# Performance work log

Measured on AMD Instinct MI355X. Metric: run time of the kernel, lower is better.

## Reference

```python
import jax, jax.numpy as jnp
import numpy as np

NUM_HEADS = 12
NUM_GROUPS = 4
METRIC_SCALE = 1.0
CLS_MIX = 1.0
MEAN_MIX = 0.5
ROUTER_SCALE = 1.0
DIFF_SCALE = 1.0
B, N, D, HF = 16, 577, 768, 3072


def _ln(x, g, b, eps=1e-5):
    mu = jnp.mean(x, axis=-1, keepdims=True)
    var = jnp.mean(jnp.square(x - mu), axis=-1, keepdims=True)
    return (x - mu) * jax.lax.rsqrt(var + eps) * g + b


def setup_inputs() -> dict:
    key = jax.random.key(0)
    ks = iter(jax.random.split(key, 16))
    w = lambda shape, std: jax.random.normal(next(ks), shape, jnp.float32) * std
    return {
        "x": w((B, N, D), 1.0),
        "ln1_g": jnp.ones((D,)), "ln1_b": jnp.zeros((D,)),
        "ad_ln_g": jnp.ones((D,)), "ad_ln_b": jnp.zeros((D,)),
        "ad_w": w((D, D), 0.02),
        "w_qkv": w((D, 3 * D), 0.02),
        "w_proj": w((D, D), 0.02), "b_proj": jnp.zeros((D,)),
        "ln2_g": jnp.ones((D,)), "ln2_b": jnp.zeros((D,)),
        "fc1_w": w((D, HF), 0.02), "fc1_b": jnp.zeros((HF,)),
        "fc2_w": w((HF, D), 0.02), "fc2_b": jnp.zeros((D,)),
        "r_ln_g": jnp.ones((HF,)), "r_ln_b": jnp.zeros((HF,)),
        "r_proj_w": w((2 * HF, NUM_GROUPS), 0.02), "r_proj_b": jnp.zeros((NUM_GROUPS,)),
        "r_gate_w": w((2 * HF, 1), 0.02), "r_gate_b": jnp.full((1,), -2.0),
        "r_scale": jnp.full((NUM_GROUPS,), 0.1),
        "d_ln_g": jnp.ones((HF,)), "d_ln_b": jnp.zeros((HF,)),
        "d_out_w": w((HF, HF), 0.005),
        "d_gate_w": w((HF, 1), 0.02), "d_gate_b": jnp.full((1,), -1.5),
    }


def reference(x, ln1_g, ln1_b, ad_ln_g, ad_ln_b, ad_w, w_qkv, w_proj, b_proj,
              ln2_g, ln2_b, fc1_w, fc1_b, fc2_w, fc2_b,
              r_ln_g, r_ln_b, r_proj_w, r_proj_b, r_gate_w, r_gate_b, r_scale,
              d_ln_g, d_ln_b, d_out_w, d_gate_w, d_gate_b):
    b, n, d = x.shape
    hd = d // NUM_HEADS
    # ---- GeoAttention (pre-norm) ----
    h = _ln(x, ln1_g, ln1_b)
    # metric adapter: residual LN+Linear (SharedAttentionMetricAdapter)
    metric_h = h + METRIC_SCALE * (_ln(h, ad_ln_g, ad_ln_b) @ ad_w)
    # q,k from metric path; v from plain path (asymmetric Q/K vs V)
    qk = metric_h @ w_qkv[:, : 2 * d]                # [b,n,2d]
    v = h @ w_qkv[:, 2 * d :]                        # [b,n,d]
    q = qk[..., :d].reshape(b, n, NUM_HEADS, hd).transpose(0, 2, 1, 3)
    k = qk[..., d:].reshape(b, n, NUM_HEADS, hd).transpose(0, 2, 1, 3)
    v = v.reshape(b, n, NUM_HEADS, hd).transpose(0, 2, 1, 3)
    attn = jax.nn.softmax(jnp.einsum("bhnd,bhmd->bhnm", q, k) * (hd ** -0.5), axis=-1)
    out = jnp.einsum("bhnm,bhmd->bhnd", attn, v).transpose(0, 2, 1, 3).reshape(b, n, d)
    x = x + out @ w_proj + b_proj
    # ---- GeoMlp (pre-norm) ----
    h2 = _ln(x, ln2_g, ln2_b)
    hid = h2 @ fc1_w + fc1_b                         # [b,n,HF]
    # GroupCompetitionRouter on hidden
    rn = _ln(hid, r_ln_g, r_ln_b)
    summary = jnp.concatenate([CLS_MIX * rn[:, 0], MEAN_MIX * jnp.mean(rn[:, 1:], axis=1)], axis=-1)  # [b,2HF]
    wts = jax.nn.softmax(summary @ r_proj_w + r_proj_b, axis=-1)       # [b,G]
    gate = jax.nn.sigmoid(summary @ r_gate_w + r_gate_b)               # [b,1]
    centered = wts * float(NUM_GROUPS) - 1.0
    grouped = hid.reshape(b, n, NUM_GROUPS, HF // NUM_GROUPS)
    scale = 1.0 + ROUTER_SCALE * gate[:, None, :, None] * r_scale[None, None, :, None] * centered[:, None, :, None]
    hid = (grouped * scale).reshape(b, n, HF)
    # TokenDiffusionMixer on hidden
    dn = _ln(hid, d_ln_g, d_ln_b)
    tr = dn / jnp.maximum(jnp.linalg.norm(dn, axis=-1, keepdims=True), 1e-12)
    aff = jax.nn.softmax(jnp.einsum("bnc,bmc->bnm", tr, tr) * (HF ** -0.5), axis=-1)
    diffusion = jnp.einsum("bnm,bmc->bnc", aff, dn) - dn
    dgate = jax.nn.sigmoid(dn[:, 0] @ d_gate_w + d_gate_b)             # [b,1]
    hid = hid + DIFF_SCALE * dgate[:, :, None] * (diffusion @ d_out_w)
    # activation + fc2
    hid = jax.nn.gelu(hid, approximate=False)
    return x + hid @ fc2_w + fc2_b
```

## Files before the change

kernel.cpp:

```cpp
#include <hip/hip_runtime.h>
#include <math.h>

typedef unsigned short u16;
typedef unsigned int   u32;
typedef __attribute__((ext_vector_type(4))) float f32x4;
typedef __attribute__((ext_vector_type(4))) u32   u32x4;
typedef __attribute__((ext_vector_type(8))) short s16x8;

#define DEV __device__ __forceinline__
#define AS1 __attribute__((address_space(1)))
#define AS3 __attribute__((address_space(3)))

DEV float b2f(u16 u){ u32 x = ((u32)u)<<16; float f; __builtin_memcpy(&f,&x,4); return f; }
DEV u16 f2b(float f){ u32 x; __builtin_memcpy(&x,&f,4); u32 r = x + 0x7FFFu + ((x>>16)&1u); return (u16)(r>>16); }

DEV float ldf(const float* p, long i){ return p[i]; }
DEV float ldf(const u16*   p, long i){ return b2f(p[i]); }

DEV void gload16(const u16* g, u16* l){
  __builtin_amdgcn_global_load_lds((const AS1 u32*)(const void*)g,
                                   (AS3 u32*)(void*)l, 16, 0, 0);
}

DEV float wave_sum(float v){
#pragma unroll
  for(int o=32;o;o>>=1) v += __shfl_down(v,o,64);
  return v;
}
DEV float wave_max(float v){
#pragma unroll
  for(int o=32;o;o>>=1) v = fmaxf(v, __shfl_down(v,o,64));
  return v;
}
DEV float block_sum(float v, float* tmp){
  v = wave_sum(v);
  if((threadIdx.x&63)==0) tmp[threadIdx.x>>6]=v;
  __syncthreads();
  float r = tmp[0]+tmp[1]+tmp[2]+tmp[3];
  __syncthreads();
  return r;
}
DEV float block_max(float v, float* tmp){
  v = wave_max(v);
  if((threadIdx.x&63)==0) tmp[threadIdx.x>>6]=v;
  __syncthreads();
  float r = fmaxf(fmaxf(tmp[0],tmp[1]),fmaxf(tmp[2],tmp[3]));
  __syncthreads();
  return r;
}

template<typename TI>
__global__ void transpose_pad(const TI* __restrict__ in, u16* __restrict__ out,
                              int R, int C, int Rpad, long strideI, long strideO){
  __shared__ u16 t[32][33];
  in  += (long)blockIdx.z*strideI;
  out += (long)blockIdx.z*strideO;
  int tx = threadIdx.x & 31, ty = threadIdx.x >> 5;
  int bc = blockIdx.x*32, br = blockIdx.y*32;
#pragma unroll
  for(int i=0;i<32;i+=8){
    int r = br+ty+i, c = bc+tx;
    float v = (r<R && c<C) ? ldf(in,(long)r*C+c) : 0.f;
    t[ty+i][tx] = f2b(v);
  }
  __syncthreads();
#pragma unroll
  for(int i=0;i<32;i+=8){
    int c = bc+ty+i, r = br+tx;
    if(c<C && r<Rpad) out[(long)c*Rpad + r] = t[tx][ty+i];
  }
}

template<typename TI>
__global__ void ln_rows(const TI* __restrict__ x, const float* __restrict__ g,
                        const float* __restrict__ b, u16* __restrict__ y, int W){
  __shared__ float tmp[4];
  long base=(long)blockIdx.x*W;
  float s=0.f, ss=0.f;
  for(int c=threadIdx.x;c<W;c+=256){ float v=ldf(x,base+c); s+=v; ss+=v*v; }
  s=block_sum(s,tmp); ss=block_sum(ss,tmp);
  float mu=s/W;
  float rstd=rsqrtf(fmaxf(ss/W-mu*mu,0.f)+1e-5f);
  for(int c=threadIdx.x;c<W;c+=256){
    float v=ldf(x,base+c);
    y[base+c]=f2b((v-mu)*rstd*g[c]+b[c]);
  }
}

__global__ void row_stats(const u16* __restrict__ x, float* __restrict__ stats, int W){
  __shared__ float tmp[4];
  long base=(long)blockIdx.x*W;
  float s=0.f,ss=0.f;
  for(int c=threadIdx.x;c<W;c+=256){ float v=b2f(x[base+c]); s+=v; ss+=v*v; }
  s=block_sum(s,tmp); ss=block_sum(ss,tmp);
  if(threadIdx.x==0){
    float mu=s/W;
    stats[2*(long)blockIdx.x]=mu;
    stats[2*(long)blockIdx.x+1]=rsqrtf(fmaxf(ss/W-mu*mu,0.f)+1e-5f);
  }
}

__global__ void dn_kernel(const u16* __restrict__ x, const float* __restrict__ g,
                          const float* __restrict__ b, const float* __restrict__ scalef,
                          u16* __restrict__ dn, float* __restrict__ rn){
  const int W=3072;
  __shared__ float tmp[4];
  __shared__ u16 rowb[3072];
  long row=(long)blockIdx.x;
  long base=row*(long)W;
  int bz=(int)(row/577);
  float s=0.f,ss=0.f;
  for(int c=threadIdx.x;c<W;c+=256){
    float sc=scalef[bz*4 + ((c>>8)/3)];
    float v=b2f(x[base+c])*sc;
    rowb[c]=f2b(v);
    s+=v; ss+=v*v;
  }
  s=block_sum(s,tmp); ss=block_sum(ss,tmp);
  float mu=s/W;
  float rstd=rsqrtf(fmaxf(ss/W-mu*mu,0.f)+1e-5f);
  float sq=0.f;
  for(int c=threadIdx.x;c<W;c+=256){
    float v=(b2f(rowb[c])-mu)*rstd*g[c]+b[c];
    sq+=v*v;
  }
  sq=block_sum(sq,tmp);
  float r=1.f/fmaxf(sqrtf(sq),1e-12f);
  for(int c=threadIdx.x;c<W;c+=256){
    float v=(b2f(rowb[c])-mu)*rstd*g[c]+b[c];
    dn[base+c]=f2b(v);
  }
  if(threadIdx.x==0) rn[blockIdx.x]=r;
}

__global__ void softmax_rows(u16* __restrict__ S, int W, int Wp,
                             const float* __restrict__ rs, int rpb, float alpha){
  __shared__ float tmp[4];
  long row = blockIdx.x;
  u16* p = S + row*(long)Wp;
  float rowscale = alpha;
  const float* rsb = nullptr;
  if(rs){ long bt=row/rpb; int m=(int)(row%rpb); rsb = rs + bt*(long)rpb; rowscale *= rsb[m]; }
  float mx=-3e38f;
  for(int c=threadIdx.x;c<W;c+=256){
    float v=b2f(p[c])*rowscale; if(rs) v*=rsb[c];
    mx=fmaxf(mx,v);
  }
  mx=block_max(mx,tmp);
  float sm=0.f;
  for(int c=threadIdx.x;c<W;c+=256){
    float v=b2f(p[c])*rowscale; if(rs) v*=rsb[c];
    sm+=__expf(v-mx);
  }
  sm=block_sum(sm,tmp);
  float inv=1.f/sm;
  for(int c=threadIdx.x;c<W;c+=256){
    float v=b2f(p[c])*rowscale; if(rs) v*=rsb[c];
    p[c]=f2b(__expf(v-mx)*inv);
  }
  for(int c=W+threadIdx.x;c<Wp;c+=256) p[c]=0;
}

__global__ void split_heads(const u16* __restrict__ qk, u16* __restrict__ qh, u16* __restrict__ kh){
  int i = blockIdx.x*256+threadIdx.x;
  if(i >= 16*577*12*8) return;
  int dv = i&7; int h=(i>>3)%12; int bn=i/96;
  int b=bn/577, n=bn%577;
  long src=(long)bn*1536 + h*64 + dv*8;
  long dst=((long)((b*12+h)*577+n))*64 + dv*8;
  *(u32x4*)(qh+dst) = *(const u32x4*)(qk+src);
  *(u32x4*)(kh+dst) = *(const u32x4*)(qk+src+768);
}
__global__ void merge_heads(const u16* __restrict__ aoh, u16* __restrict__ aout){
  int i = blockIdx.x*256+threadIdx.x;
  if(i >= 16*577*12*8) return;
  int dv=i&7; int h=(i>>3)%12; int bn=i/96;
  int b=bn/577, n=bn%577;
  long dst=(long)bn*768 + h*64 + dv*8;
  long src=((long)((b*12+h)*577+n))*64 + dv*8;
  *(u32x4*)(aout+dst) = *(const u32x4*)(aoh+src);
}
__global__ void make_vT(const u16* __restrict__ v, u16* __restrict__ vT){
  long i = (long)blockIdx.x*256+threadIdx.x;
  if(i >= (long)192*64*608) return;
  int n=(int)(i%608); long q=i/608; int d=(int)(q&63); int bh=(int)(q>>6);
  int b=bh/12, h=bh%12;
  u16 val=0;
  if(n<577) val = v[((long)(b*577+n))*768 + h*64 + d];
  vT[i]=val;
}

__global__ void summary_kernel(const u16* __restrict__ hid, const float* __restrict__ stats,
                               const float* __restrict__ rg, const float* __restrict__ rb,
                               float* __restrict__ summ){
  int b=blockIdx.y;
  int c=blockIdx.x*256+threadIdx.x;
  const u16* hb=hid+(size_t)b*577*3072;
  const float* st=stats+(size_t)b*577*2;
  float g=rg[c], be=rb[c];
  float cls=(b2f(hb[c])-st[0])*st[1]*g+be;
  float acc=0.f;
  for(int n=1;n<577;n++) acc += (b2f(hb[(size_t)n*3072+c])-st[2*n])*st[2*n+1];
  summ[(size_t)b*6144+c]        = 1.0f*cls;
  summ[(size_t)b*6144+3072+c]   = 0.5f*(g*(acc*(1.f/576.f))+be);
}

__global__ void router_kernel(const float* __restrict__ summ, const float* __restrict__ pw,
                              const float* __restrict__ pb, const float* __restrict__ gw,
                              const float* __restrict__ gb, const float* __restrict__ rsc,
                              float* __restrict__ scalef){
  __shared__ float tmp[4];
  int b=blockIdx.x;
  float a0=0,a1=0,a2=0,a3=0,a4=0;
  for(int c=threadIdx.x;c<6144;c+=256){
    float sv=summ[(size_t)b*6144+c];
    a0+=sv*pw[c*4+0]; a1+=sv*pw[c*4+1]; a2+=sv*pw[c*4+2]; a3+=sv*pw[c*4+3];
    a4+=sv*gw[c];
  }
  a0=block_sum(a0,tmp); a1=block_sum(a1,tmp); a2=block_sum(a2,tmp);
  a3=block_sum(a3,tmp); a4=block_sum(a4,tmp);
  if(threadIdx.x==0){
    float l0=a0+pb[0], l1=a1+pb[1], l2=a2+pb[2], l3=a3+pb[3];
    float mx=fmaxf(fmaxf(l0,l1),fmaxf(l2,l3));
    float e0=__expf(l0-mx),e1=__expf(l1-mx),e2=__expf(l2-mx),e3=__expf(l3-mx);
    float s=e0+e1+e2+e3;
    float gate=1.f/(1.f+__expf(-(a4+gb[0])));
    float w0=e0/s,w1=e1/s,w2=e2/s,w3=e3/s;
    scalef[b*4+0]=1.f+gate*rsc[0]*(4.f*w0-1.f);
    scalef[b*4+1]=1.f+gate*rsc[1]*(4.f*w1-1.f);
    scalef[b*4+2]=1.f+gate*rsc[2]*(4.f*w2-1.f);
    scalef[b*4+3]=1.f+gate*rsc[3]*(4.f*w3-1.f);
  }
}

__global__ void dgate_kernel(const u16* __restrict__ dn, const float* __restrict__ gw,
                             const float* __restrict__ gb, float* __restrict__ dgate){
  __shared__ float tmp[4];
  int b=blockIdx.x;
  const u16* row = dn + (size_t)b*577*3072;
  float a=0.f;
  for(int c=threadIdx.x;c<3072;c+=256) a+=b2f(row[c])*gw[c];
  a=block_sum(a,tmp);
  if(threadIdx.x==0) dgate[b]=1.f/(1.f+__expf(-(a+gb[0])));
}

constexpr int F_BIAS=1, F_RES=2, F_GELU=4, F_GATE=8, F_RESF32=16, F_OUTF32=32, F_SCRES=64;

DEV int swz(int u){ int row=u>>2, sl=u&3; return row*4 + (sl ^ ((row>>1)&3)); }

template<int FLAGS>
__global__ __launch_bounds__(256,2) void gemm_bt(
  const u16* __restrict__ A, long lda, long szA,
  const u16* __restrict__ B, long ldb, long szB,
  void* __restrict__ Cv, long ldc, long szC,
  const float* __restrict__ bias,
  const void* __restrict__ resv, long ldr, long szR, float res_scale,
  const float* __restrict__ gate,
  float alpha, int M, int N, int K, int NX, int NY)
{
  __shared__ alignas(16) u16 shA[128*32];
  __shared__ alignas(16) u16 shB[128*32];
  const int nwg = (int)gridDim.x;
  const int orig = (int)blockIdx.x;
  const int q = nwg>>3, r = nwg&7;
  const int xcd = orig&7, idx = orig>>3;
  const int wg = (xcd<r ? xcd*(q+1) : r*(q+1)+(xcd-r)*q) + idx;
  const int by = wg % NY; const int t_ = wg / NY;
  const int bx = t_ % NX; const int z  = t_ / NX;

  A += (long)z*szA; B += (long)z*szB;
  const int tid=threadIdx.x, lane=tid&63, wid=tid>>6;
  const int wr=wid>>1, wc=wid&1;
  const long m0=(long)bx*128, n0=(long)by*128;
  f32x4 acc[4][4];
#pragma unroll
  for(int i=0;i<4;i++)
#pragma unroll
    for(int j=0;j<4;j++){ f32x4 zv={0.f,0.f,0.f,0.f}; acc[i][j]=zv; }

  const int lr = lane>>2, lsl = lane&3;
  const u16* pA[2]; const u16* pB[2]; u16* lA[2]; u16* lB[2];
#pragma unroll
  for(int i=0;i<2;i++){
    int ra = wid*32 + i*16 + lr;
    int kc = (lsl ^ ((ra>>1)&3))*8;
    long gr = m0+ra; if(gr>=M) gr=M-1;
    long gb = n0+ra; if(gb>=N) gb=N-1;
    pA[i] = A + gr*lda + kc;
    pB[i] = B + gb*ldb + kc;
    lA[i] = shA + (wid*32 + i*16)*32;
    lB[i] = shB + (wid*32 + i*16)*32;
  }

  for(int k0=0;k0<K;k0+=32){
    __syncthreads();
#pragma unroll
    for(int i=0;i<2;i++){
      gload16(pA[i]+k0, lA[i]);
      gload16(pB[i]+k0, lB[i]);
    }
    __syncthreads();
    const int ks = lane>>4, rr = lane&15;
    s16x8 av[4], bv[4];
#pragma unroll
    for(int mi=0;mi<4;mi++) av[mi] = ((const s16x8*)shA)[swz((wr*64+mi*16+rr)*4+ks)];
#pragma unroll
    for(int ni=0;ni<4;ni++) bv[ni] = ((const s16x8*)shB)[swz((wc*64+ni*16+rr)*4+ks)];
#pragma unroll
    for(int mi=0;mi<4;mi++)
#pragma unroll
      for(int ni=0;ni<4;ni++)
        acc[mi][ni] = __builtin_amdgcn_mfma_f32_16x16x32_bf16(av[mi], bv[ni], acc[mi][ni], 0,0,0);
  }
  const float* resf = (const float*)resv + (long)z*szR;
  const u16*   resh = (const u16*)resv   + (long)z*szR;
  float* Cf = (float*)Cv + (long)z*szC;
  u16*   Ch = (u16*)Cv   + (long)z*szC;
  float gv = (FLAGS&F_GATE)? gate[z] : 1.f;
#pragma unroll
  for(int mi=0;mi<4;mi++){
#pragma unroll
    for(int ni=0;ni<4;ni++){
      long c0 = n0 + wc*64 + ni*16 + (lane&15);
      if(c0>=N) continue;
      float bb = (FLAGS&F_BIAS)? bias[c0] : 0.f;
#pragma unroll
      for(int r2=0;r2<4;r2++){
        long rw = m0 + wr*64 + mi*16 + (lane>>4)*4 + r2;
        if(rw>=M) continue;
        float t = acc[mi][ni][r2]*alpha*gv + bb;
        if(FLAGS&F_RES){
          float rvv = (FLAGS&F_RESF32)? resf[rw*ldr+c0] : b2f(resh[rw*ldr+c0]);
          t += res_scale*rvv;
        }
        if(FLAGS&F_GELU) t = 0.5f*t*(1.f+erff(t*0.70710678118654752f));
        if(FLAGS&F_OUTF32) Cf[rw*ldc+c0]=t;
        else               Ch[rw*ldc+c0]=f2b(t);
      }
    }
  }
}

static inline int gpack(int M,int N,int nb,int& NX,int& NY){
  NX=(M+127)/128; NY=(N+127)/128; return NX*NY*nb;
}

template<int FLAGS>
__global__ __launch_bounds__(512,2) void gemm256(
  const u16* __restrict__ A, long lda,
  const u16* __restrict__ B, long ldb,
  void* __restrict__ Cv, long ldc,
  const float* __restrict__ bias,
  const void* __restrict__ resv, long ldr,
  const float* __restrict__ gate, const float* __restrict__ scres,
  float irpz, float alpha, int M, int N, int K, int NY)
{
  __shared__ alignas(16) u16 smem[65536];
  char* sm=(char*)smem;
  const int nwg=(int)gridDim.x, orig=(int)blockIdx.x;
  const int qq=nwg>>3, rr8=nwg&7, xcd=orig&7, idx=orig>>3;
  const int wg=(xcd<rr8? xcd*(qq+1): rr8*(qq+1)+(xcd-rr8)*qq)+idx;
  const int by=wg%NY, bx=wg/NY;
  const long m0=(long)bx*256, n0=(long)by*256;
  const int tid=threadIdx.x, lane=tid&63, wid=tid>>6;
  const int wr=wid>>2, wc=wid&3, l15=lane&15, ks=lane>>4;

  f32x4 acc[8][4];
#pragma unroll
  for(int i=0;i<8;i++)
#pragma unroll
    for(int j=0;j<4;j++){ f32x4 zv={0.f,0.f,0.f,0.f}; acc[i][j]=zv; }

  const u16 *sA[2][2], *sB[2][2];
  int dstj[2];
#pragma unroll
  for(int j=0;j<2;j++){
    int u=j*512+tid, row=u>>3;
    long co=(long)(((u&7)^(row&7))*8);
    dstj[j]=u*16;
#pragma unroll
    for(int h=0;h<2;h++){
      long gr=m0+h*128+row; if(gr>=M) gr=M-1;
      long gb=n0+h*128+row; if(gb>=N) gb=N-1;
      sA[h][j]=A+gr*lda+co;
      sB[h][j]=B+gb*ldb+co;
    }
  }
  int xsl[2]; xsl[0]=((ks^(l15&7))<<4); xsl[1]=(((4+ks)^(l15&7))<<4);
  const int arow = wr*16384 + l15*128;
  int brow[4];
#pragma unroll
  for(int nj=0;nj<4;nj++){ int n=wc*64+nj*16; brow[nj]=32768+(n>>7)*16384+((n&127)+l15)*128; }
  const int NT=K>>6;

#define STG(P,mat,h,kt,bf) { \
  gload16(P[h][0]+(long)(kt)*64,(u16*)(sm+(bf)*65536+(mat)*32768+(h)*16384+dstj[0])); \
  gload16(P[h][1]+(long)(kt)*64,(u16*)(sm+(bf)*65536+(mat)*32768+(h)*16384+dstj[1])); }
#define BAR() { asm volatile("":::"memory"); __builtin_amdgcn_s_barrier(); asm volatile("":::"memory"); }
#define LGKM() { asm volatile("s_waitcnt lgkmcnt(0)":::"memory"); __builtin_amdgcn_sched_barrier(0); }
#define MFMA16(A0,KB) { \
  __builtin_amdgcn_s_setprio(1); \
  _Pragma("unroll") for(int i_=0;i_<4;i_++) \
  _Pragma("unroll") for(int j_=0;j_<4;j_++) \
    acc[(A0)+i_][j_] = __builtin_amdgcn_mfma_f32_16x16x32_bf16(av[i_], bv[KB][j_], acc[(A0)+i_][j_], 0,0,0); \
  __builtin_amdgcn_s_setprio(0); }

  STG(sA,0,0,0,0); STG(sA,0,1,0,0); STG(sB,1,0,0,0); STG(sB,1,1,0,0);
  STG(sB,1,0,1,1); STG(sB,1,1,1,1);
  asm volatile("s_waitcnt vmcnt(4)":::"memory");
  BAR();

  s16x8 av[4], bv[2][4];
  for(int t=0;t<NT;++t){
    const int cur=t&1, nxt=cur^1;
    const char* bp = sm + cur*65536;
#pragma unroll
    for(int kk=0;kk<2;kk++)
#pragma unroll
      for(int nj=0;nj<4;nj++) bv[kk][nj]=*(const s16x8*)(bp+brow[nj]+xsl[kk]);
#pragma unroll
    for(int i=0;i<4;i++) av[i]=*(const s16x8*)(bp+arow+i*2048+xsl[0]);
    if(t+1<NT){ STG(sA,0,0,t+1,nxt); STG(sA,0,1,t+1,nxt); }
    BAR();
    LGKM();
    MFMA16(0,0);
    BAR();
#pragma unroll
    for(int i=0;i<4;i++) av[i]=*(const s16x8*)(bp+arow+(4+i)*2048+xsl[0]);
    BAR();
    LGKM();
    MFMA16(4,0);
    BAR();
#pragma unroll
    for(int i=0;i<4;i++) av[i]=*(const s16x8*)(bp+arow+i*2048+xsl[1]);
    if(t+2<NT) STG(sB,1,0,t+2,cur);
    BAR();
    LGKM();
    MFMA16(0,1);
    BAR();
#pragma unroll
    for(int i=0;i<4;i++) av[i]=*(const s16x8*)(bp+arow+(4+i)*2048+xsl[1]);
    if(t+2<NT) STG(sB,1,1,t+2,cur);
    if(t+2<NT) asm volatile("s_waitcnt vmcnt(4)":::"memory");
    else       asm volatile("s_waitcnt vmcnt(0)":::"memory");
    BAR();
    LGKM();
    MFMA16(4,1);
    BAR();
  }
#undef STG
#undef BAR
#undef LGKM
#undef MFMA16

  const float* resf=(const float*)resv; const u16* resh=(const u16*)resv;
  float* Cf=(float*)Cv; u16* Ch=(u16*)Cv;
#pragma unroll
  for(int mf=0;mf<8;mf++){
#pragma unroll
    for(int j=0;j<4;j++){
      long c0 = n0 + wc*64 + j*16 + l15;
      float bb=(FLAGS&F_BIAS)? bias[c0]:0.f;
      int cg=((int)(c0>>8))/3;
#pragma unroll
      for(int r2=0;r2<4;r2++){
        long rw = m0 + wr*128 + mf*16 + ks*4 + r2;
        if(rw>=M) continue;
        float t=acc[mf][j][r2]*alpha;
        if(FLAGS&(F_GATE|F_SCRES)){
          int z=(int)(((float)rw+0.5f)*irpz);
          if(FLAGS&F_GATE) t*=gate[z];
          if(FLAGS&F_SCRES) t += scres[z*4+cg]*b2f(resh[rw*ldr+c0]);
        } else if(FLAGS&F_RES){
          float rvv=(FLAGS&F_RESF32)? resf[rw*ldr+c0] : b2f(resh[rw*ldr+c0]);
          t += rvv;
        }
        t+=bb;
        if(FLAGS&F_GELU) t=0.5f*t*(1.f+erff(t*0.70710678118654752f));
        if(FLAGS&F_OUTF32) Cf[rw*ldc+c0]=t;
        else               Ch[rw*ldc+c0]=f2b(t);
      }
    }
  }
}

extern "C" void kernel_launch(void* const* d_in, const int* in_sizes, int n_in,
                              void* d_out, int out_size, void* d_ws, size_t ws_size,
                              hipStream_t stream){
  const int BNr=16*577;
  const float* x      = (const float*)d_in[0];
  const float* ln1_g  = (const float*)d_in[1];
  const float* ln1_b  = (const float*)d_in[2];
  const float* ad_ln_g= (const float*)d_in[3];
  const float* ad_ln_b= (const float*)d_in[4];
  const float* ad_w   = (const float*)d_in[5];
  const float* w_qkv  = (const float*)d_in[6];
  const float* w_proj = (const float*)d_in[7];
  const float* b_proj = (const float*)d_in[8];
  const float* ln2_g  = (const float*)d_in[9];
  const float* ln2_b  = (const float*)d_in[10];
  const float* fc1_w  = (const float*)d_in[11];
  const float* fc1_b  = (const float*)d_in[12];
  const float* fc2_w  = (const float*)d_in[13];
  const float* fc2_b  = (const float*)d_in[14];
  const float* r_ln_g = (const float*)d_in[15];
  const float* r_ln_b = (const float*)d_in[16];
  const float* r_proj_w=(const float*)d_in[17];
  const float* r_proj_b=(const float*)d_in[18];
  const float* r_gate_w=(const float*)d_in[19];
  const float* r_gate_b=(const float*)d_in[20];
  const float* r_scale =(const float*)d_in[21];
  const float* d_ln_g = (const float*)d_in[22];
  const float* d_ln_b = (const float*)d_in[23];
  const float* d_outw = (const float*)d_in[24];
  const float* d_gate_w=(const float*)d_in[25];
  const float* d_gate_b=(const float*)d_in[26];

  char* ws=(char*)d_ws;
  size_t off=0;
  auto take=[&](size_t nb){ size_t r=off; off=(off+nb+255)&~(size_t)255; return r; };
  auto al  =[&](size_t v){ return (v+255)&~(size_t)255; };
  const size_t o_qkvT = take((size_t)2304*768*2);
  const size_t o_adT  = take((size_t)768*768*2);
  const size_t o_projT= take((size_t)768*768*2);
  const size_t o_fc1T = take((size_t)3072*768*2);
  const size_t o_fc2T = take((size_t)768*3072*2);
  const size_t o_doutT= take((size_t)3072*3072*2);
  const size_t o_x2   = take((size_t)BNr*768*4);
  const size_t o_hid  = take((size_t)BNr*3072*2);
  const size_t o_stats= take((size_t)BNr*2*4);
  const size_t o_rn   = take((size_t)BNr*4);
  const size_t o_sum  = take((size_t)16*6144*4);
  const size_t o_scalef=take(64*4);
  const size_t o_dg   = take(64);
  const size_t o_h    = take((size_t)BNr*768*2);
  const size_t o_lnh  = take((size_t)BNr*768*2);
  const size_t o_metric=take((size_t)BNr*768*2);
  const size_t o_qk   = take((size_t)BNr*1536*2);
  const size_t o_v    = take((size_t)BNr*768*2);
  const size_t o_qh   = take((size_t)192*577*64*2);
  const size_t o_kh   = take((size_t)192*577*64*2);
  const size_t o_vT   = take((size_t)192*64*608*2);
  (void)o_v; (void)o_vT; (void)ws_size; (void)in_sizes; (void)n_in; (void)out_size;
  const size_t o_S    = o_qk;
  const size_t o_aoh  = o_metric;
  const size_t o_aout = o_h;
  const size_t o_h2   = o_lnh;
  const size_t o_dn   = o_h;
  const size_t o_aff  = al(o_dn + (size_t)BNr*3072*2);
  const size_t o_dnTb = al(o_aff + (size_t)16*577*608*2);
  const size_t o_diff = al(o_dnTb + (size_t)4*3072*608*2);
  const size_t o_hact = o_dn;

  u16* qkvT=(u16*)(ws+o_qkvT); u16* adT=(u16*)(ws+o_adT); u16* projT=(u16*)(ws+o_projT);
  u16* fc1T=(u16*)(ws+o_fc1T); u16* fc2T=(u16*)(ws+o_fc2T); u16* doutT=(u16*)(ws+o_doutT);
  float* x2=(float*)(ws+o_x2); u16* hid=(u16*)(ws+o_hid);
  float* stats=(float*)(ws+o_stats); float* rn=(float*)(ws+o_rn);
  float* summ=(float*)(ws+o_sum); float* scalef=(float*)(ws+o_scalef); float* dgate=(float*)(ws+o_dg);
  u16* hbuf=(u16*)(ws+o_h); u16* lnh=(u16*)(ws+o_lnh); u16* metric=(u16*)(ws+o_metric);
  u16* qkbuf=(u16*)(ws+o_qk); u16* vbuf=(u16*)(ws+o_v);
  u16* qh=(u16*)(ws+o_qh); u16* kh=(u16*)(ws+o_kh); u16* vT=(u16*)(ws+o_vT);
  u16* Sc=(u16*)(ws+o_S); u16* aoh=(u16*)(ws+o_aoh); u16* aout=(u16*)(ws+o_aout);
  u16* h2=(u16*)(ws+o_h2);
  u16* dn=(u16*)(ws+o_dn); u16* aff=(u16*)(ws+o_aff); u16* dnTb=(u16*)(ws+o_dnTb);
  u16* diff=(u16*)(ws+o_diff); u16* hact=(u16*)(ws+o_hact);

  dim3 blk(256), blk5(512);
  int NX, NY, ng;
  transpose_pad<float><<<dim3(72,24,1),blk,0,stream>>>(w_qkv, qkvT, 768,2304,768, 0,0);
  transpose_pad<float><<<dim3(24,24,1),blk,0,stream>>>(ad_w,  adT,  768,768, 768, 0,0);
  transpose_pad<float><<<dim3(24,24,1),blk,0,stream>>>(w_proj,projT,768,768, 768, 0,0);
  transpose_pad<float><<<dim3(96,24,1),blk,0,stream>>>(fc1_w, fc1T, 768,3072,768, 0,0);
  transpose_pad<float><<<dim3(24,96,1),blk,0,stream>>>(fc2_w, fc2T, 3072,768,3072,0,0);
  transpose_pad<float><<<dim3(96,96,1),blk,0,stream>>>(d_outw,doutT,3072,3072,3072,0,0);
  ln_rows<float><<<BNr,blk,0,stream>>>(x, ln1_g, ln1_b, hbuf, 768);
  ln_rows<u16>  <<<BNr,blk,0,stream>>>(hbuf, ad_ln_g, ad_ln_b, lnh, 768);
  ng=gpack(BNr,768,1,NX,NY);
  gemm_bt<F_RES><<<ng,blk,0,stream>>>(lnh,768,0, adT,768,0, metric,768,0,
      nullptr, hbuf,768,0, 1.f, nullptr, 1.f, BNr,768,768, NX,NY);
  gemm256<0><<<dim3(37*6),blk5,0,stream>>>(metric,768, qkvT,768, qkbuf,1536,
      nullptr, nullptr,0, nullptr,nullptr, 0.f, 1.f, BNr,1536,768, 6);
  ng=gpack(BNr,768,1,NX,NY);
  gemm_bt<0><<<ng,blk,0,stream>>>(hbuf,768,0, qkvT+(size_t)1536*768,768,0, vbuf,768,0,
      nullptr, nullptr,0,0,0.f, nullptr, 1.f, BNr,768,768, NX,NY);
  split_heads<<<3462,blk,0,stream>>>(qkbuf, qh, kh);
  make_vT<<<29184,blk,0,stream>>>(vbuf, vT);
  for(int c=0;c<6;c++){
    const u16* qc=qh+(size_t)c*32*577*64;
    const u16* kc=kh+(size_t)c*32*577*64;
    ng=gpack(577,577,32,NX,NY);
    gemm_bt<0><<<ng,blk,0,stream>>>(qc,64,(long)577*64, kc,64,(long)577*64,
        Sc,608,(long)577*608, nullptr, nullptr,0,0,0.f, nullptr, 0.125f, 577,577,64, NX,NY);
    softmax_rows<<<32*577,blk,0,stream>>>(Sc,577,608, nullptr,577, 1.f);
    ng=gpack(577,64,32,NX,NY);
    gemm_bt<0><<<ng,blk,0,stream>>>(Sc,608,(long)577*608, vT+(size_t)c*32*64*608,608,(long)64*608,
        aoh+(size_t)c*32*577*64,64,(long)577*64, nullptr, nullptr,0,0,0.f, nullptr, 1.f, 577,64,608, NX,NY);
  }
  merge_heads<<<3462,blk,0,stream>>>(aoh, aout);
  ng=gpack(BNr,768,1,NX,NY);
  gemm_bt<F_RES|F_BIAS|F_RESF32|F_OUTF32><<<ng,blk,0,stream>>>(aout,768,0, projT,768,0,
      x2,768,0, b_proj, x,768,0, 1.f, nullptr, 1.f, BNr,768,768, NX,NY);
  ln_rows<float><<<BNr,blk,0,stream>>>(x2, ln2_g, ln2_b, h2, 768);
  gemm256<F_BIAS><<<dim3(37*12),blk5,0,stream>>>(h2,768, fc1T,768, hid,3072,
      fc1_b, nullptr,0, nullptr,nullptr, 0.f, 1.f, BNr,3072,768, 12);
  row_stats<<<BNr,blk,0,stream>>>(hid, stats, 3072);
  summary_kernel<<<dim3(12,16),blk,0,stream>>>(hid, stats, r_ln_g, r_ln_b, summ);
  router_kernel<<<16,blk,0,stream>>>(summ, r_proj_w, r_proj_b, r_gate_w, r_gate_b, r_scale, scalef);
  dn_kernel<<<BNr,blk,0,stream>>>(hid, d_ln_g, d_ln_b, scalef, dn, rn);
  dgate_kernel<<<16,blk,0,stream>>>(dn, d_gate_w, d_gate_b, dgate);
  ng=gpack(577,577,16,NX,NY);
  gemm_bt<0><<<ng,blk,0,stream>>>(dn,3072,(long)577*3072, dn,3072,(long)577*3072,
      aff,608,(long)577*608, nullptr, nullptr,0,0,0.f, nullptr, 1.f, 577,577,3072, NX,NY);
  softmax_rows<<<BNr,blk,0,stream>>>(aff,577,608, rn,577, 0.01804219634f);
  for(int g4=0; g4<4; ++g4){
    transpose_pad<u16><<<dim3(96,19,4),blk,0,stream>>>(dn+(size_t)g4*4*577*3072, dnTb,
        577,3072,608, (long)577*3072, (long)3072*608);
    ng=gpack(577,3072,4,NX,NY);
    gemm_bt<F_RES><<<ng,blk,0,stream>>>(aff+(size_t)g4*4*577*608,608,(long)577*608,
        dnTb,608,(long)3072*608, diff+(size_t)g4*4*577*3072,3072,(long)577*3072,
        nullptr, dn+(size_t)g4*4*577*3072,3072,(long)577*3072, -1.f, nullptr, 1.f, 577,3072,608, NX,NY);
  }
  gemm256<F_GELU|F_GATE|F_SCRES><<<dim3(37*12),blk5,0,stream>>>(diff,3072, doutT,3072,
      hact,3072, nullptr, hid,3072, dgate, scalef, 1.f/577.f, 1.f, BNr,3072,3072, 12);
  ng=gpack(BNr,768,1,NX,NY);
  gemm_bt<F_RES|F_BIAS|F_RESF32|F_OUTF32><<<ng,blk,0,stream>>>(hact,3072,0,
      fc2T,3072,0, d_out,768,0, fc2_b, x2,768,0, 1.f, nullptr, 1.f, BNr,768,3072, NX,NY);
}
```

Before: 1.512 ms.

## Batch attention and diffusion GEMMs into single launches when workspace allows

When the workspace is large enough, the six per-chunk attention launches (QK^T, softmax, PV) and the four diffusion transpose+GEMM chunks are each replaced by one launch over all heads or batches. The goal is to cut launch count and the tail underutilisation of small grids. It also fuses the two back-to-back layernorms into one kernel that keeps the row in shared memory, and unrolls the summary reduction loop. The cost is a much larger scratch buffer for the full score and transposed tensors; if the workspace is too small, the chunked path is used as a fallback.

```diff
diff --git a/kernel.cpp b/kernel.cpp
--- a/kernel.cpp
+++ b/kernel.cpp
@@ -84,6 +84,32 @@
   for(int c=threadIdx.x;c<W;c+=256){
     float v=ldf(x,base+c);
     y[base+c]=f2b((v-mu)*rstd*g[c]+b[c]);
+  }
+}
+
+__global__ void ln2_rows(const float* __restrict__ x,
+                         const float* __restrict__ g1, const float* __restrict__ b1,
+                         const float* __restrict__ g2, const float* __restrict__ b2,
+                         u16* __restrict__ h, u16* __restrict__ lnh){
+  __shared__ float tmp[4];
+  __shared__ float row[768];
+  long base=(long)blockIdx.x*768;
+  float s=0.f, ss=0.f;
+  for(int c=threadIdx.x;c<768;c+=256){ float v=x[base+c]; s+=v; ss+=v*v; }
+  s=block_sum(s,tmp); ss=block_sum(ss,tmp);
+  float mu=s*(1.f/768.f);
+  float rstd=rsqrtf(fmaxf(ss*(1.f/768.f)-mu*mu,0.f)+1e-5f);
+  float s2=0.f, ss2=0.f;
+  for(int c=threadIdx.x;c<768;c+=256){
+    float v=(x[base+c]-mu)*rstd*g1[c]+b1[c];
+    row[c]=v; h[base+c]=f2b(v);
+    s2+=v; ss2+=v*v;
+  }
+  s2=block_sum(s2,tmp); ss2=block_sum(ss2,tmp);
+  float mu2=s2*(1.f/768.f);
+  float rstd2=rsqrtf(fmaxf(ss2*(1.f/768.f)-mu2*mu2,0.f)+1e-5f);
+  for(int c=threadIdx.x;c<768;c+=256){
+    lnh[base+c]=f2b((row[c]-mu2)*rstd2*g2[c]+b2[c]);
   }
 }
 
@@ -200,6 +226,7 @@
   float g=rg[c], be=rb[c];
   float cls=(b2f(hb[c])-st[0])*st[1]*g+be;
   float acc=0.f;
+#pragma unroll 4
   for(int n=1;n<577;n++) acc += (b2f(hb[(size_t)n*3072+c])-st[2*n])*st[2*n+1];
   summ[(size_t)b*6144+c]        = 1.0f*cls;
   summ[(size_t)b*6144+3072+c]   = 0.5f*(g*(acc*(1.f/576.f))+be);
@@ -541,7 +568,7 @@
   const size_t o_qh   = take((size_t)192*577*64*2);
   const size_t o_kh   = take((size_t)192*577*64*2);
   const size_t o_vT   = take((size_t)192*64*608*2);
-  (void)o_v; (void)o_vT; (void)ws_size; (void)in_sizes; (void)n_in; (void)out_size;
+  (void)o_v; (void)o_vT; (void)in_sizes; (void)n_in; (void)out_size;
   const size_t o_S    = o_qk;
   const size_t o_aoh  = o_metric;
   const size_t o_aout = o_h;
@@ -551,6 +578,11 @@
   const size_t o_dnTb = al(o_aff + (size_t)16*577*608*2);
   const size_t o_diff = al(o_dnTb + (size_t)4*3072*608*2);
   const size_t o_hact = o_dn;
+  size_t endA = off;
+  size_t endB = o_diff + (size_t)BNr*3072*2;
+  const size_t o_big = al(endA > endB ? endA : endB);
+  const size_t big_need = (size_t)192*577*608*2;
+  const bool bigws = ws_size >= o_big + big_need;
 
   u16* qkvT=(u16*)(ws+o_qkvT); u16* adT=(u16*)(ws+o_adT); u16* projT=(u16*)(ws+o_projT);
   u16* fc1T=(u16*)(ws+o_fc1T); u16* fc2T=(u16*)(ws+o_fc2T); u16* doutT=(u16*)(ws+o_doutT);
@@ -564,6 +596,7 @@
   u16* h2=(u16*)(ws+o_h2);
   u16* dn=(u16*)(ws+o_dn); u16* aff=(u16*)(ws+o_aff); u16* dnTb=(u16*)(ws+o_dnTb);
   u16* diff=(u16*)(ws+o_diff); u16* hact=(u16*)(ws+o_hact);
+  u16* Sf=(u16*)(ws+o_big); u16* dnTbF=(u16*)(ws+o_big);
 
   dim3 blk(256), blk5(512);
   int NX, NY, ng;
@@ -573,8 +606,7 @@
   transpose_pad<float><<<dim3(96,24,1),blk,0,stream>>>(fc1_w, fc1T, 768,3072,768, 0,0);
   transpose_pad<float><<<dim3(24,96,1),blk,0,stream>>>(fc2_w, fc2T, 3072,768,3072,0,0);
   transpose_pad<float><<<dim3(96,96,1),blk,0,stream>>>(d_outw,doutT,3072,3072,3072,0,0);
-  ln_rows<float><<<BNr,blk,0,stream>>>(x, ln1_g, ln1_b, hbuf, 768);
-  ln_rows<u16>  <<<BNr,blk,0,stream>>>(hbuf, ad_ln_g, ad_ln_b, lnh, 768);
+  ln2_rows<<<BNr,blk,0,stream>>>(x, ln1_g, ln1_b, ad_ln_g, ad_ln_b, hbuf, lnh);
   ng=gpack(BNr,768,1,NX,NY);
   gemm_bt<F_RES><<<ng,blk,0,stream>>>(lnh,768,0, adT,768,0, metric,768,0,
       nullptr, hbuf,768,0, 1.f, nullptr, 1.f, BNr,768,768, NX,NY);
@@ -585,16 +617,26 @@
       nullptr, nullptr,0,0,0.f, nullptr, 1.f, BNr,768,768, NX,NY);
   split_heads<<<3462,blk,0,stream>>>(qkbuf, qh, kh);
   make_vT<<<29184,blk,0,stream>>>(vbuf, vT);
-  for(int c=0;c<6;c++){
-    const u16* qc=qh+(size_t)c*32*577*64;
-    const u16* kc=kh+(size_t)c*32*577*64;
-    ng=gpack(577,577,32,NX,NY);
-    gemm_bt<0><<<ng,blk,0,stream>>>(qc,64,(long)577*64, kc,64,(long)577*64,
-        Sc,608,(long)577*608, nullptr, nullptr,0,0,0.f, nullptr, 0.125f, 577,577,64, NX,NY);
-    softmax_rows<<<32*577,blk,0,stream>>>(Sc,577,608, nullptr,577, 1.f);
-    ng=gpack(577,64,32,NX,NY);
-    gemm_bt<0><<<ng,blk,0,stream>>>(Sc,608,(long)577*608, vT+(size_t)c*32*64*608,608,(long)64*608,
-        aoh+(size_t)c*32*577*64,64,(long)577*64, nullptr, nullptr,0,0,0.f, nullptr, 1.f, 577,64,608, NX,NY);
+  if(bigws){
+    ng=gpack(577,577,192,NX,NY);
+    gemm_bt<0><<<ng,blk,0,stream>>>(qh,64,(long)577*64, kh,64,(long)577*64,
+        Sf,608,(long)577*608, nullptr, nullptr,0,0,0.f, nullptr, 0.125f, 577,577,64, NX,NY);
+    softmax_rows<<<192*577,blk,0,stream>>>(Sf,577,608, nullptr,577, 1.f);
+    ng=gpack(577,64,192,NX,NY);
+    gemm_bt<0><<<ng,blk,0,stream>>>(Sf,608,(long)577*608, vT,608,(long)64*608,
+        aoh,64,(long)577*64, nullptr, nullptr,0,0,0.f, nullptr, 1.f, 577,64,608, NX,NY);
+  } else {
+    for(int c=0;c<6;c++){
+      const u16* qc=qh+(size_t)c*32*577*64;
+      const u16* kc=kh+(size_t)c*32*577*64;
+      ng=gpack(577,577,32,NX,NY);
+      gemm_bt<0><<<ng,blk,0,stream>>>(qc,64,(long)577*64, kc,64,(long)577*64,
+          Sc,608,(long)577*608, nullptr, nullptr,0,0,0.f, nullptr, 0.125f, 577,577,64, NX,NY);
+      softmax_rows<<<32*577,blk,0,stream>>>(Sc,577,608, nullptr,577, 1.f);
+      ng=gpack(577,64,32,NX,NY);
+      gemm_bt<0><<<ng,blk,0,stream>>>(Sc,608,(long)577*608, vT+(size_t)c*32*64*608,608,(long)64*608,
+          aoh+(size_t)c*32*577*64,64,(long)577*64, nullptr, nullptr,0,0,0.f, nullptr, 1.f, 577,64,608, NX,NY);
+    }
   }
   merge_heads<<<3462,blk,0,stream>>>(aoh, aout);
   ng=gpack(BNr,768,1,NX,NY);
@@ -612,13 +654,22 @@
   gemm_bt<0><<<ng,blk,0,stream>>>(dn,3072,(long)577*3072, dn,3072,(long)577*3072,
       aff,608,(long)577*608, nullptr, nullptr,0,0,0.f, nullptr, 1.f, 577,577,3072, NX,NY);
   softmax_rows<<<BNr,blk,0,stream>>>(aff,577,608, rn,577, 0.01804219634f);
-  for(int g4=0; g4<4; ++g4){
-    transpose_pad<u16><<<dim3(96,19,4),blk,0,stream>>>(dn+(size_t)g4*4*577*3072, dnTb,
+  if(bigws){
+    transpose_pad<u16><<<dim3(96,19,16),blk,0,stream>>>(dn, dnTbF,
         577,3072,608, (long)577*3072, (long)3072*608);
-    ng=gpack(577,3072,4,NX,NY);
-    gemm_bt<F_RES><<<ng,blk,0,stream>>>(aff+(size_t)g4*4*577*608,608,(long)577*608,
-        dnTb,608,(long)3072*608, diff+(size_t)g4*4*577*3072,3072,(long)577*3072,
-        nullptr, dn+(size_t)g4*4*577*3072,3072,(long)577*3072, -1.f, nullptr, 1.f, 577,3072,608, NX,NY);
+    ng=gpack(577,3072,16,NX,NY);
+    gemm_bt<F_RES><<<ng,blk,0,stream>>>(aff,608,(long)577*608,
+        dnTbF,608,(long)3072*608, diff,3072,(long)577*3072,
+        nullptr, dn,3072,(long)577*3072, -1.f, nullptr, 1.f, 577,3072,608, NX,NY);
+  } else {
+    for(int g4=0; g4<4; ++g4){
+      transpose_pad<u16><<<dim3(96,19,4),blk,0,stream>>>(dn+(size_t)g4*4*577*3072, dnTb,
+          577,3072,608, (long)577*3072, (long)3072*608);
+      ng=gpack(577,3072,4,NX,NY);
+      gemm_bt<F_RES><<<ng,blk,0,stream>>>(aff+(size_t)g4*4*577*608,608,(long)577*608,
+          dnTb,608,(long)3072*608, diff+(size_t)g4*4*577*3072,3072,(long)577*3072,
+          nullptr, dn+(size_t)g4*4*577*3072,3072,(long)577*3072, -1.f, nullptr, 1.f, 577,3072,608, NX,NY);
+    }
   }
   gemm256<F_GELU|F_GATE|F_SCRES><<<dim3(37*12),blk5,0,stream>>>(diff,3072, doutT,3072,
       hact,3072, nullptr, hid,3072, dgate, scalef, 1.f/577.f, 1.f, BNr,3072,3072, 12);
```

Result: no change. 1.530 ms (+1.2%).
